# Kernel tuning notes

Hardware: AMD Instinct MI355X
Metric: run time of the kernel (lower is better)

## Reference

```python
import jax, jax.numpy as jnp
import numpy as np

EMBED_DIM = 256
B, H, S = 8, 20, 1024


def setup_inputs() -> dict:
    key = jax.random.key(0)
    ks = jax.random.split(key, 10)
    E = EMBED_DIM
    d2, d4 = 2 * E, 4 * E

    def lin(kw, kb, out_dim, in_dim):
        bound = 1.0 / np.sqrt(in_dim)
        w = jax.random.uniform(kw, (out_dim, in_dim), minval=-bound, maxval=bound, dtype=jnp.float32)
        b = jax.random.uniform(kb, (out_dim,), minval=-bound, maxval=bound, dtype=jnp.float32)
        return w, b

    wc_w, wc_b = lin(ks[0], ks[1], d2, d2)
    wh_w, wh_b = lin(ks[2], ks[3], d2, d2)
    qt_w, qt_b = lin(ks[4], ks[5], 1, d2)
    wf_w, wf_b = lin(ks[6], ks[7], E, d4)

    hist = jax.random.normal(ks[8], (B, H, S, d2), dtype=jnp.float32)
    cur = jax.random.normal(ks[9], (B, S, d2), dtype=jnp.float32)
    return {
        "wca_history_embeddings": hist,
        "wca_current_embeddings": cur,
        "wc_w": wc_w, "wc_b": wc_b,
        "wh_w": wh_w, "wh_b": wh_b,
        "qt_w": qt_w, "qt_b": qt_b,
        "wf_w": wf_w, "wf_b": wf_b,
    }


def reference(wca_history_embeddings, wca_current_embeddings,
              wc_w, wc_b, wh_w, wh_b, qt_w, qt_b, wf_w, wf_b):
    # hist: [B, H, S, 2E]; cur: [B, S, 2E]
    c_proj = jnp.einsum('bsd,ed->bse', wca_current_embeddings, wc_w) + wc_b   # [B,S,2E]
    h_proj = jnp.einsum('bhsd,ed->bhse', wca_history_embeddings, wh_w) + wh_b  # [B,H,S,2E]
    gate = jax.nn.sigmoid(c_proj[:, None, :, :] + h_proj)                      # [B,H,S,2E]
    # alpha[b,h,s] = qt(gate) -- raw scores, NO softmax (matches original)
    alpha = jnp.einsum('bhse,e->bhs', gate, qt_w[0]) + qt_b[0]                 # [B,H,S]
    # weighted neighbor sum over history dim
    summed = jnp.einsum('bhs,bhsd->bsd', alpha, wca_history_embeddings)        # [B,S,2E]
    fused = jnp.concatenate([wca_current_embeddings, summed], axis=-1)         # [B,S,4E]
    final = jnp.einsum('bsd,ed->bse', fused, wf_w) + wf_b                      # [B,S,E]
    return final
```

## Files before the change

kernel.cpp:

```cpp
#include <hip/hip_runtime.h>
#include <hip/hip_bf16.h>
#include <stdint.h>

static constexpr int Bn = 8, Hn = 20, Sn = 1024, En = 256, D2 = 512, D4 = 1024;
static constexpr int Mall = Bn * Hn * Sn;
static constexpr int BS   = Bn * Sn;

typedef __attribute__((ext_vector_type(8))) short bf16x8;
typedef __attribute__((ext_vector_type(4))) float f32x4;

__device__ __forceinline__ unsigned short f2bf(float f) {
  unsigned int u = __float_as_uint(f);
  u += 0x7FFFu + ((u >> 16) & 1u);
  return (unsigned short)(u >> 16);
}
__device__ __forceinline__ float bf2f(unsigned short u) {
  return __uint_as_float(((unsigned int)u) << 16);
}
__device__ __forceinline__ float sigmoid_fast(float x) {
  return __builtin_amdgcn_rcpf(1.0f + __expf(-x));
}
__device__ __forceinline__ unsigned int packbf_trunc(float a, float b) {
  return __builtin_amdgcn_perm(__float_as_uint(b), __float_as_uint(a),
                               0x07060302u);
}
__device__ __forceinline__ unsigned int packbf_rne(float a, float b) {
  return ((unsigned int)f2bf(b) << 16) | (unsigned int)f2bf(a);
}
__device__ __forceinline__ uint4 pack8_trunc(float4 f0, float4 f1) {
  uint4 p;
  p.x = packbf_trunc(f0.x, f0.y);
  p.y = packbf_trunc(f0.z, f0.w);
  p.z = packbf_trunc(f1.x, f1.y);
  p.w = packbf_trunc(f1.z, f1.w);
  return p;
}

typedef const __attribute__((address_space(1))) void gv_t;
typedef __attribute__((address_space(3))) void lv_t;
__device__ __forceinline__ void gload_lds16(const void* g, void* l) {
  __builtin_amdgcn_global_load_lds((gv_t*)g, (lv_t*)l, 16, 0, 0);
}

__global__ __launch_bounds__(256) void k_convert_weights(
    const float* __restrict__ wc, const float* __restrict__ wh,
    const float* __restrict__ wf,
    unsigned short* __restrict__ wcb, unsigned short* __restrict__ whb,
    unsigned short* __restrict__ wfb) {
  int idx4 = blockIdx.x * 256 + threadIdx.x;
  int a = idx4 >> 16;
  int r = idx4 & 65535;
  const float* s = (a == 0) ? wc : (a == 1) ? wh : wf;
  unsigned short* d = (a == 0) ? wcb : (a == 1) ? whb : wfb;
  float4 v = reinterpret_cast<const float4*>(s)[r];
  ushort4 o;
  o.x = f2bf(v.x); o.y = f2bf(v.y); o.z = f2bf(v.z); o.w = f2bf(v.w);
  reinterpret_cast<ushort4*>(d)[r] = o;
}

template <int MODE>
__global__ __launch_bounds__(256) void k_gemm_bt(
    const float* __restrict__ A,
    const unsigned short* __restrict__ Bw,
    const float* __restrict__ bias,
    const unsigned short* __restrict__ cproj,
    const float* __restrict__ qtw,
    const float* __restrict__ qtb,
    unsigned short* __restrict__ cproj_out,
    float* __restrict__ alpha_out) {
  __shared__ __align__(16) unsigned char ldsA[128 * 128];
  __shared__ __align__(16) unsigned char ldsB[128 * 128];

  const int tid = threadIdx.x;
  const int lane = tid & 63, wave = tid >> 6;
  const int lrow = lane & 15, lk = lane >> 4;
  const int row0 = blockIdx.x * 128;
  const f32x4 zero4 = {0.f, 0.f, 0.f, 0.f};

  float asum[2][4];
  if (MODE == 1) {
#pragma unroll
    for (int rf = 0; rf < 2; ++rf)
#pragma unroll
      for (int r = 0; r < 4; ++r) asum[rf][r] = 0.f;
  }

  const int nc_begin = (MODE == 0) ? blockIdx.y : 0;
  const int nc_end   = (MODE == 0) ? (int)blockIdx.y + 1 : 4;

  for (int nc = nc_begin; nc < nc_end; ++nc) {
    f32x4 acc[2][8];
#pragma unroll
    for (int rf = 0; rf < 2; ++rf)
#pragma unroll
      for (int cf = 0; cf < 8; ++cf) acc[rf][cf] = zero4;

    for (int kt = 0; kt < 8; ++kt) {
      __syncthreads();
#pragma unroll
      for (int slot = 0; slot < 4; ++slot) {
        int idx = (slot * 256 + tid) * 8;
        int row = idx >> 6, k = idx & 63;
        const float* src = A + (size_t)(row0 + row) * 512 + kt * 64 + k;
        float4 f0 = *reinterpret_cast<const float4*>(src);
        float4 f1 = *reinterpret_cast<const float4*>(src + 4);
        uint4 p = pack8_trunc(f0, f1);
        int off = row * 128 + ((k * 2) ^ ((row & 7) << 4));
        *reinterpret_cast<uint4*>(ldsA + off) = p;
      }
#pragma unroll
      for (int c = 0; c < 4; ++c) {
        int ci = c * 256 + tid;
        int n = ci >> 3, kc = (ci & 7) * 8;
        const unsigned short* src =
            Bw + (size_t)(nc * 128 + n) * 512 + kt * 64 + kc;
        uint4 p = *reinterpret_cast<const uint4*>(src);
        int off = n * 128 + ((kc * 2) ^ ((n & 7) << 4));
        *reinterpret_cast<uint4*>(ldsB + off) = p;
      }
      __syncthreads();
#pragma unroll
      for (int ks = 0; ks < 2; ++ks) {
        int kbyte = ks * 64 + lk * 16;
        bf16x8 af[2];
#pragma unroll
        for (int rf = 0; rf < 2; ++rf) {
          int ar = wave * 32 + rf * 16 + lrow;
          af[rf] = *reinterpret_cast<const bf16x8*>(
              ldsA + ar * 128 + (kbyte ^ ((ar & 7) << 4)));
        }
#pragma unroll
        for (int cf = 0; cf < 8; ++cf) {
          int br = cf * 16 + lrow;
          bf16x8 bf = *reinterpret_cast<const bf16x8*>(
              ldsB + br * 128 + (kbyte ^ ((br & 7) << 4)));
#pragma unroll
          for (int rf = 0; rf < 2; ++rf)
            acc[rf][cf] = __builtin_amdgcn_mfma_f32_16x16x32_bf16(
                af[rf], bf, acc[rf][cf], 0, 0, 0);
        }
      }
    }

    if (MODE == 0) {
#pragma unroll
      for (int cf = 0; cf < 8; ++cf) {
        int e = nc * 128 + cf * 16 + lrow;
        float bse = bias[e];
#pragma unroll
        for (int rf = 0; rf < 2; ++rf)
#pragma unroll
          for (int r = 0; r < 4; ++r) {
            int row = row0 + wave * 32 + rf * 16 + lk * 4 + r;
            cproj_out[(size_t)row * 512 + e] = f2bf(acc[rf][cf][r] + bse);
          }
      }
    } else {
#pragma unroll
      for (int cf = 0; cf < 8; ++cf) {
        int e = nc * 128 + cf * 16 + lrow;
        float whb = bias[e];
        float qw = qtw[e];
#pragma unroll
        for (int rf = 0; rf < 2; ++rf)
#pragma unroll
          for (int r = 0; r < 4; ++r) {
            int row = row0 + wave * 32 + rf * 16 + lk * 4 + r;
            int bsrow = ((row / (Hn * Sn)) << 10) | (row & 1023);
            float cp = bf2f(cproj[(size_t)bsrow * 512 + e]);
            float g = sigmoid_fast(acc[rf][cf][r] + whb + cp);
            asum[rf][r] = fmaf(g, qw, asum[rf][r]);
          }
      }
    }
  }

  if (MODE == 1) {
#pragma unroll
    for (int off = 1; off < 16; off <<= 1) {
#pragma unroll
      for (int rf = 0; rf < 2; ++rf)
#pragma unroll
        for (int r = 0; r < 4; ++r)
          asum[rf][r] += __shfl_xor(asum[rf][r], off, 64);
    }
    if (lrow == 0) {
      float qb = qtb[0];
#pragma unroll
      for (int rf = 0; rf < 2; ++rf)
#pragma unroll
        for (int r = 0; r < 4; ++r) {
          int row = row0 + wave * 32 + rf * 16 + lk * 4 + r;
          alpha_out[row] = asum[rf][r] + qb;
        }
    }
  }
}

__global__ __launch_bounds__(256, 1) void k_alpha_summed(
    const float* __restrict__ A,
    const unsigned short* __restrict__ Bw,
    const float* __restrict__ bias,
    const unsigned short* __restrict__ cproj,
    const float* __restrict__ qtw,
    const float* __restrict__ qtb,
    unsigned short* __restrict__ summed) {
  __shared__ __align__(16) unsigned char ldsA[81920];
  __shared__ __align__(16) unsigned char ldsB[65536];
  __shared__ __align__(16) unsigned char ldsC[4096];

  const int tid = threadIdx.x;
  const int lane = tid & 63, wave = tid >> 6;
  const int lrow = lane & 15, lk = lane >> 4;
  const int wc = wave;
  const int b = blockIdx.x >> 8;
  const int s0 = (blockIdx.x & 255) * 4;
  const size_t rowbase = (size_t)b * 20480;
  const f32x4 zero4 = {0.f, 0.f, 0.f, 0.f};

  float4 pa[5];
  auto issueA = [&](int sl) {
#pragma unroll
    for (int j = 0; j < 5; ++j) {
      int f = j * 256 + tid;
      int mr = f >> 4, q = f & 15;
      pa[j] = *reinterpret_cast<const float4*>(
          A + (rowbase + (size_t)(mr >> 2) * 1024 + s0 + (mr & 3)) * 512 +
          sl * 64 + q * 4);
    }
  };
  auto writeA = [&](int sl) {
#pragma unroll
    for (int j = 0; j < 5; ++j) {
      int f = j * 256 + tid;
      int mr = f >> 4, q = f & 15;
      unsigned int u0 = packbf_rne(pa[j].x, pa[j].y);
      unsigned int u1 = packbf_rne(pa[j].z, pa[j].w);
      int g = sl * 8 + (q >> 1);
      int off = mr * 1024 + ((g ^ (mr & 7)) << 4) + ((q & 1) << 3);
      *reinterpret_cast<uint2*>(ldsA + off) = make_uint2(u0, u1);
    }
  };

  const int brow = tid >> 3;
  const int bslot = (tid & 7) ^ (brow & 7);
  const unsigned short* gB0 = Bw + (size_t)brow * 512 + bslot * 8;
  char* lB = (char*)ldsB + wave * 1024;

  {
    const unsigned short* csrc = cproj + ((size_t)b * 1024 + s0) * 512;
    gload_lds16(csrc + tid * 8, (char*)ldsC + wave * 1024);
  }
  issueA(0); writeA(0);
  issueA(1); writeA(1);

  f32x4 acc[5][8];
#pragma unroll
  for (int tm = 0; tm < 5; ++tm)
#pragma unroll
    for (int n = 0; n < 8; ++n) acc[tm][n] = zero4;

  for (int kt = 0; kt < 8; ++kt) {
    __syncthreads();
#pragma unroll
    for (int j = 0; j < 16; ++j)
      gload_lds16(gB0 + j * 16384 + kt * 64, lB + j * 4096);
    __builtin_amdgcn_sched_barrier(0);
    if (kt < 6) {
      issueA(kt + 2);
      __builtin_amdgcn_sched_barrier(0);
      asm volatile("s_waitcnt vmcnt(5)" ::: "memory");
    } else {
      asm volatile("s_waitcnt vmcnt(0)" ::: "memory");
    }
    __builtin_amdgcn_s_barrier();
    __builtin_amdgcn_sched_barrier(0);
#pragma unroll
    for (int ks = 0; ks < 2; ++ks) {
      bf16x8 af[5];
#pragma unroll
      for (int tm = 0; tm < 5; ++tm) {
        int r = tm * 16 + lrow;
        int g = (kt * 8 + ks * 4 + lk) ^ (r & 7);
        af[tm] = *reinterpret_cast<const bf16x8*>(ldsA + r * 1024 + g * 16);
      }
#pragma unroll
      for (int n = 0; n < 8; ++n) {
        int r = wc * 128 + n * 16 + lrow;
        int slot = (ks * 4 + lk) ^ (r & 7);
        bf16x8 bv =
            *reinterpret_cast<const bf16x8*>(ldsB + r * 128 + slot * 16);
#pragma unroll
        for (int tm = 0; tm < 5; ++tm)
          acc[tm][n] = __builtin_amdgcn_mfma_f32_16x16x32_bf16(af[tm], bv,
                                                               acc[tm][n], 0,
                                                               0, 0);
      }
    }
    if (kt < 6) writeA(kt + 2);
  }

  float asum[5][4];
#pragma unroll
  for (int tm = 0; tm < 5; ++tm)
#pragma unroll
    for (int r = 0; r < 4; ++r) asum[tm][r] = 0.f;

  const unsigned short* cpl = reinterpret_cast<const unsigned short*>(ldsC);
#pragma unroll
  for (int n = 0; n < 8; ++n) {
    int e = wc * 128 + n * 16 + lrow;
    float whb = bias[e];
    float qw = qtw[e];
    float cpv[4];
#pragma unroll
    for (int si = 0; si < 4; ++si) cpv[si] = bf2f(cpl[si * 512 + e]);
#pragma unroll
    for (int tm = 0; tm < 5; ++tm)
#pragma unroll
      for (int r = 0; r < 4; ++r) {
        float g = sigmoid_fast(acc[tm][n][r] + whb + cpv[r]);
        asum[tm][r] = fmaf(g, qw, asum[tm][r]);
      }
  }
#pragma unroll
  for (int off = 1; off < 16; off <<= 1)
#pragma unroll
    for (int tm = 0; tm < 5; ++tm)
#pragma unroll
      for (int r = 0; r < 4; ++r)
        asum[tm][r] += __shfl_xor(asum[tm][r], off, 64);

  __syncthreads();
  float* red = reinterpret_cast<float*>(ldsC);
  if (lrow == 0) {
#pragma unroll
    for (int tm = 0; tm < 5; ++tm)
#pragma unroll
      for (int r = 0; r < 4; ++r)
        red[wc * 80 + tm * 16 + lk * 4 + r] = asum[tm][r];
  }
  __syncthreads();

  const int si = wave;
  const float qb = qtb[0];
  float o[8];
#pragma unroll
  for (int j = 0; j < 8; ++j) o[j] = 0.f;
#pragma unroll
  for (int h = 0; h < 20; ++h) {
    int mr = h * 4 + si;
    float a = red[mr] + red[80 + mr] + red[160 + mr] + red[240 + mr] + qb;
    int g = lane ^ (mr & 7);
    bf16x8 av = *reinterpret_cast<const bf16x8*>(ldsA + mr * 1024 + g * 16);
#pragma unroll
    for (int j = 0; j < 8; ++j)
      o[j] = fmaf(a, bf2f((unsigned short)av[j]), o[j]);
  }
  uint4 pk;
  pk.x = packbf_rne(o[0], o[1]);
  pk.y = packbf_rne(o[2], o[3]);
  pk.z = packbf_rne(o[4], o[5]);
  pk.w = packbf_rne(o[6], o[7]);
  size_t orow = (size_t)b * 1024 + s0 + si;
  reinterpret_cast<uint4*>(summed)[orow * 64 + lane] = pk;
}

__global__ __launch_bounds__(256) void k_summed(
    const float* __restrict__ hist, const float* __restrict__ alpha,
    unsigned short* __restrict__ summed) {
  int idx = blockIdx.x * 256 + threadIdx.x;
  int bs = idx >> 7, c4 = idx & 127;
  int b = bs >> 10, s = bs & 1023;
  const float4* hp = reinterpret_cast<const float4*>(hist);
  float4 acc = make_float4(0.f, 0.f, 0.f, 0.f);
#pragma unroll
  for (int h = 0; h < Hn; ++h) {
    int bh = b * Hn + h;
    float a = alpha[(bh << 10) + s];
    float4 v = hp[(size_t)(bh * 1024 + s) * 128 + c4];
    acc.x = fmaf(a, v.x, acc.x);
    acc.y = fmaf(a, v.y, acc.y);
    acc.z = fmaf(a, v.z, acc.z);
    acc.w = fmaf(a, v.w, acc.w);
  }
  ushort4 o;
  o.x = f2bf(acc.x); o.y = f2bf(acc.y); o.z = f2bf(acc.z); o.w = f2bf(acc.w);
  reinterpret_cast<ushort4*>(summed)[idx] = o;
}

__global__ __launch_bounds__(256) void k_final(
    const float* __restrict__ cur,
    const unsigned short* __restrict__ summed,
    const unsigned short* __restrict__ wfb16,
    const float* __restrict__ wf_bias,
    float* __restrict__ out) {
  __shared__ __align__(16) unsigned char ldsA[64 * 128];
  __shared__ __align__(16) unsigned char ldsB[128 * 128];
  const int tid = threadIdx.x;
  const int lane = tid & 63, wave = tid >> 6;
  const int lrow = lane & 15, lk = lane >> 4;
  const int row0 = blockIdx.x * 64;
  const int n0 = blockIdx.y * 128;
  const f32x4 zero4 = {0.f, 0.f, 0.f, 0.f};

  f32x4 acc[8];
#pragma unroll
  for (int cf = 0; cf < 8; ++cf) acc[cf] = zero4;

  for (int kt = 0; kt < 16; ++kt) {
    __syncthreads();
#pragma unroll
    for (int slot = 0; slot < 2; ++slot) {
      int idx = (slot * 256 + tid) * 8;
      int row = idx >> 6, k = idx & 63;
      int gcol = kt * 64 + k;
      uint4 p;
      if (kt < 8) {
        const float* src = cur + (size_t)(row0 + row) * 512 + gcol;
        float4 f0 = *reinterpret_cast<const float4*>(src);
        float4 f1 = *reinterpret_cast<const float4*>(src + 4);
        p = pack8_trunc(f0, f1);
      } else {
        p = *reinterpret_cast<const uint4*>(
            summed + (size_t)(row0 + row) * 512 + gcol - 512);
      }
      int off = row * 128 + ((k * 2) ^ ((row & 7) << 4));
      *reinterpret_cast<uint4*>(ldsA + off) = p;
    }
#pragma unroll
    for (int c = 0; c < 4; ++c) {
      int ci = c * 256 + tid;
      int n = ci >> 3, kc = (ci & 7) * 8;
      uint4 p = *reinterpret_cast<const uint4*>(
          wfb16 + (size_t)(n0 + n) * 1024 + kt * 64 + kc);
      int off = n * 128 + ((kc * 2) ^ ((n & 7) << 4));
      *reinterpret_cast<uint4*>(ldsB + off) = p;
    }
    __syncthreads();
#pragma unroll
    for (int ks = 0; ks < 2; ++ks) {
      int kbyte = ks * 64 + lk * 16;
      int ar = wave * 16 + lrow;
      bf16x8 a = *reinterpret_cast<const bf16x8*>(
          ldsA + ar * 128 + (kbyte ^ ((ar & 7) << 4)));
#pragma unroll
      for (int cf = 0; cf < 8; ++cf) {
        int br = cf * 16 + lrow;
        bf16x8 b = *reinterpret_cast<const bf16x8*>(
            ldsB + br * 128 + (kbyte ^ ((br & 7) << 4)));
        acc[cf] = __builtin_amdgcn_mfma_f32_16x16x32_bf16(a, b, acc[cf], 0, 0, 0);
      }
    }
  }
#pragma unroll
  for (int cf = 0; cf < 8; ++cf) {
    int col = n0 + cf * 16 + lrow;
    float bse = wf_bias[col];
#pragma unroll
    for (int r = 0; r < 4; ++r) {
      int row = row0 + wave * 16 + lk * 4 + r;
      out[(size_t)row * 256 + col] = acc[cf][r] + bse;
    }
  }
}

extern "C" void kernel_launch(void* const* d_in, const int* in_sizes, int n_in,
                              void* d_out, int out_size, void* d_ws,
                              size_t ws_size, hipStream_t stream) {
  (void)in_sizes; (void)n_in; (void)out_size;
  const float* hist = (const float*)d_in[0];
  const float* cur  = (const float*)d_in[1];
  const float* wc_w = (const float*)d_in[2];
  const float* wc_b = (const float*)d_in[3];
  const float* wh_w = (const float*)d_in[4];
  const float* wh_b = (const float*)d_in[5];
  const float* qt_w = (const float*)d_in[6];
  const float* qt_b = (const float*)d_in[7];
  const float* wf_w = (const float*)d_in[8];
  const float* wf_b = (const float*)d_in[9];
  float* out = (float*)d_out;
  char* ws = (char*)d_ws;

  unsigned short* wcb    = (unsigned short*)(ws);
  unsigned short* whb    = (unsigned short*)(ws + 524288);
  unsigned short* wfb    = (unsigned short*)(ws + 1048576);
  unsigned short* cproj  = (unsigned short*)(ws + 1572864);
  float*          alpha  = (float*)(ws + 9961472);
  unsigned short* summed = (unsigned short*)(ws + 10616832);
  const size_t NEED = 19005440;

  k_convert_weights<<<dim3(768), dim3(256), 0, stream>>>(wc_w, wh_w, wf_w, wcb,
                                                         whb, wfb);
  k_gemm_bt<0><<<dim3(BS / 128, 4), dim3(256), 0, stream>>>(
      cur, wcb, wc_b, nullptr, nullptr, nullptr, cproj, nullptr);
  if (ws_size >= NEED) {
    k_alpha_summed<<<dim3(2048), dim3(256), 0, stream>>>(
        hist, whb, wh_b, cproj, qt_w, qt_b, summed);
  } else {
    k_gemm_bt<1><<<dim3(Mall / 128, 1), dim3(256), 0, stream>>>(
        hist, whb, wh_b, cproj, qt_w, qt_b, nullptr, alpha);
    k_summed<<<dim3(4096), dim3(256), 0, stream>>>(hist, alpha, summed);
  }
  k_final<<<dim3(BS / 64, 2), dim3(256), 0, stream>>>(cur, summed, wfb, wf_b,
                                                      out);
}
```

Before: 273.2 us.

## Split fused alpha kernel across eight waves with double-buffered half-K weight pipeline

The fused alpha/summed kernel goes from 256 to 512 threads. Each of the eight waves now owns 64 output columns instead of 128. The weight tile is staged in 32-wide K slices into a double-buffered LDS region, and the loop is unrolled into 16 explicit steps with hand-tuned vmcnt waits that interleave the next weight and history loads with compute. The goal is better latency hiding and more waves to overlap global loads with MFMA, at the cost of twice as many barriers and a wider cross-wave reduction over eight partial sums.

```diff
diff --git a/kernel.cpp b/kernel.cpp
--- a/kernel.cpp
+++ b/kernel.cpp
@@ -197,7 +197,7 @@
   }
 }
 
-__global__ __launch_bounds__(256, 1) void k_alpha_summed(
+__global__ __launch_bounds__(512, 2) void k_alpha_summed(
     const float* __restrict__ A,
     const unsigned short* __restrict__ Bw,
     const float* __restrict__ bias,
@@ -218,98 +218,124 @@
   const size_t rowbase = (size_t)b * 20480;
   const f32x4 zero4 = {0.f, 0.f, 0.f, 0.f};
 
-  float4 pa[5];
-  auto issueA = [&](int sl) {
-#pragma unroll
-    for (int j = 0; j < 5; ++j) {
-      int f = j * 256 + tid;
-      int mr = f >> 4, q = f & 15;
-      pa[j] = *reinterpret_cast<const float4*>(
-          A + (rowbase + (size_t)(mr >> 2) * 1024 + s0 + (mr & 3)) * 512 +
-          sl * 64 + q * 4);
+  const unsigned short* gB0 =
+      Bw + (size_t)(lane >> 2) * 512 + ((lane & 3) ^ ((lane >> 3) & 3)) * 8;
+
+  float4 paA[3], paB[3];
+  auto issueA = [&](int t, float4 (&pa)[3]) {
+#pragma unroll
+    for (int j = 0; j < 3; ++j) {
+      if (j < 2 || tid < 256) {
+        int u = j * 512 + tid;
+        int mr = u >> 4, q = u & 15;
+        pa[j] = *reinterpret_cast<const float4*>(
+            A + (rowbase + (size_t)(mr >> 2) * 1024 + s0 + (mr & 3)) * 512 +
+            t * 64 + q * 4);
+      }
     }
   };
-  auto writeA = [&](int sl) {
-#pragma unroll
-    for (int j = 0; j < 5; ++j) {
-      int f = j * 256 + tid;
-      int mr = f >> 4, q = f & 15;
-      unsigned int u0 = packbf_rne(pa[j].x, pa[j].y);
-      unsigned int u1 = packbf_rne(pa[j].z, pa[j].w);
-      int g = sl * 8 + (q >> 1);
-      int off = mr * 1024 + ((g ^ (mr & 7)) << 4) + ((q & 1) << 3);
-      *reinterpret_cast<uint2*>(ldsA + off) = make_uint2(u0, u1);
+  auto writeA = [&](int t, float4 (&pa)[3]) {
+#pragma unroll
+    for (int j = 0; j < 3; ++j) {
+      if (j < 2 || tid < 256) {
+        int u = j * 512 + tid;
+        int mr = u >> 4, q = u & 15;
+        unsigned int u0 = packbf_rne(pa[j].x, pa[j].y);
+        unsigned int u1 = packbf_rne(pa[j].z, pa[j].w);
+        int g = t * 8 + (q >> 1);
+        int off = mr * 1024 + ((g ^ (mr & 7)) << 4) + ((q & 1) << 3);
+        *reinterpret_cast<uint2*>(ldsA + off) = make_uint2(u0, u1);
+      }
     }
   };
-
-  const int brow = tid >> 3;
-  const int bslot = (tid & 7) ^ (brow & 7);
-  const unsigned short* gB0 = Bw + (size_t)brow * 512 + bslot * 8;
-  char* lB = (char*)ldsB + wave * 1024;
-
-  {
+  auto issueB = [&](int t) {
+#pragma unroll
+    for (int j = 0; j < 4; ++j)
+      gload_lds16(gB0 + (size_t)(j * 8 + wave) * 8192 + t * 32,
+                  (char*)ldsB + (t & 1) * 32768 + (j * 8 + wave) * 1024);
+  };
+
+  f32x4 acc[5][4];
+#pragma unroll
+  for (int tm = 0; tm < 5; ++tm)
+#pragma unroll
+    for (int n = 0; n < 4; ++n) acc[tm][n] = zero4;
+
+  auto compute = [&](int k) {
+    const int kt = k >> 1, ks = k & 1;
+    bf16x8 af[5];
+#pragma unroll
+    for (int tm = 0; tm < 5; ++tm) {
+      int r = tm * 16 + lrow;
+      int g = (kt * 8 + ks * 4 + lk) ^ (r & 7);
+      af[tm] = *reinterpret_cast<const bf16x8*>(ldsA + r * 1024 + g * 16);
+    }
+    const unsigned char* bbase = ldsB + (k & 1) * 32768;
+#pragma unroll
+    for (int n = 0; n < 4; ++n) {
+      int r = wc * 64 + n * 16 + lrow;
+      int slot = lk ^ ((r >> 1) & 3);
+      bf16x8 bv = *reinterpret_cast<const bf16x8*>(bbase + r * 64 + slot * 16);
+#pragma unroll
+      for (int tm = 0; tm < 5; ++tm)
+        acc[tm][n] = __builtin_amdgcn_mfma_f32_16x16x32_bf16(af[tm], bv,
+                                                             acc[tm][n], 0, 0,
+                                                             0);
+    }
+  };
+
+  if (wave < 4) {
     const unsigned short* csrc = cproj + ((size_t)b * 1024 + s0) * 512;
     gload_lds16(csrc + tid * 8, (char*)ldsC + wave * 1024);
   }
-  issueA(0); writeA(0);
-  issueA(1); writeA(1);
-
-  f32x4 acc[5][8];
+  issueA(0, paA);
+  issueA(1, paB);
+  writeA(0, paA);
+  writeA(1, paB);
+  issueB(0);
+  issueB(1);
+  issueA(2, paA);
+
+#define KSTEP(K, VM, ...)                                        \
+  {                                                              \
+    asm volatile("s_waitcnt " VM ::: "memory");                  \
+    __builtin_amdgcn_s_barrier();                                \
+    __builtin_amdgcn_sched_barrier(0);                           \
+    compute(K);                                                  \
+    asm volatile("s_waitcnt lgkmcnt(0)" ::: "memory");           \
+    __builtin_amdgcn_s_barrier();                                \
+    __builtin_amdgcn_sched_barrier(0);                           \
+    __VA_ARGS__                                                  \
+  }
+
+  KSTEP(0, "vmcnt(6) lgkmcnt(0)", issueB(2); issueA(3, paB);)
+  KSTEP(1, "vmcnt(8)",  issueB(3);  writeA(2, paA);)
+  KSTEP(2, "vmcnt(6)",  issueB(4);  issueA(4, paA);)
+  KSTEP(3, "vmcnt(6)",  issueB(5);  writeA(3, paB);)
+  KSTEP(4, "vmcnt(6)",  issueB(6);  issueA(5, paB);)
+  KSTEP(5, "vmcnt(6)",  issueB(7);  writeA(4, paA);)
+  KSTEP(6, "vmcnt(6)",  issueB(8);  issueA(6, paA);)
+  KSTEP(7, "vmcnt(6)",  issueB(9);  writeA(5, paB);)
+  KSTEP(8, "vmcnt(6)",  issueB(10); issueA(7, paB);)
+  KSTEP(9, "vmcnt(6)",  issueB(11); writeA(6, paA);)
+  KSTEP(10, "vmcnt(6)", issueB(12);)
+  KSTEP(11, "vmcnt(4)", issueB(13); writeA(7, paB);)
+  KSTEP(12, "vmcnt(4)", issueB(14);)
+  KSTEP(13, "vmcnt(4)", issueB(15);)
+  KSTEP(14, "vmcnt(4)", )
+  KSTEP(15, "vmcnt(0)", )
+#undef KSTEP
+
+  float asum[5][4];
 #pragma unroll
   for (int tm = 0; tm < 5; ++tm)
 #pragma unroll
-    for (int n = 0; n < 8; ++n) acc[tm][n] = zero4;
-
-  for (int kt = 0; kt < 8; ++kt) {
-    __syncthreads();
-#pragma unroll
-    for (int j = 0; j < 16; ++j)
-      gload_lds16(gB0 + j * 16384 + kt * 64, lB + j * 4096);
-    __builtin_amdgcn_sched_barrier(0);
-    if (kt < 6) {
-      issueA(kt + 2);
-      __builtin_amdgcn_sched_barrier(0);
-      asm volatile("s_waitcnt vmcnt(5)" ::: "memory");
-    } else {
-      asm volatile("s_waitcnt vmcnt(0)" ::: "memory");
-    }
-    __builtin_amdgcn_s_barrier();
-    __builtin_amdgcn_sched_barrier(0);
-#pragma unroll
-    for (int ks = 0; ks < 2; ++ks) {
-      bf16x8 af[5];
-#pragma unroll
-      for (int tm = 0; tm < 5; ++tm) {
-        int r = tm * 16 + lrow;
-        int g = (kt * 8 + ks * 4 + lk) ^ (r & 7);
-        af[tm] = *reinterpret_cast<const bf16x8*>(ldsA + r * 1024 + g * 16);
-      }
-#pragma unroll
-      for (int n = 0; n < 8; ++n) {
-        int r = wc * 128 + n * 16 + lrow;
-        int slot = (ks * 4 + lk) ^ (r & 7);
-        bf16x8 bv =
-            *reinterpret_cast<const bf16x8*>(ldsB + r * 128 + slot * 16);
-#pragma unroll
-        for (int tm = 0; tm < 5; ++tm)
-          acc[tm][n] = __builtin_amdgcn_mfma_f32_16x16x32_bf16(af[tm], bv,
-                                                               acc[tm][n], 0,
-                                                               0, 0);
-      }
-    }
-    if (kt < 6) writeA(kt + 2);
-  }
-
-  float asum[5][4];
-#pragma unroll
-  for (int tm = 0; tm < 5; ++tm)
-#pragma unroll
     for (int r = 0; r < 4; ++r) asum[tm][r] = 0.f;
 
   const unsigned short* cpl = reinterpret_cast<const unsigned short*>(ldsC);
 #pragma unroll
-  for (int n = 0; n < 8; ++n) {
-    int e = wc * 128 + n * 16 + lrow;
+  for (int n = 0; n < 4; ++n) {
+    int e = wc * 64 + n * 16 + lrow;
     float whb = bias[e];
     float qw = qtw[e];
     float cpv[4];
@@ -331,8 +357,7 @@
       for (int r = 0; r < 4; ++r)
         asum[tm][r] += __shfl_xor(asum[tm][r], off, 64);
 
-  __syncthreads();
-  float* red = reinterpret_cast<float*>(ldsC);
+  float* red = reinterpret_cast<float*>(ldsB);
   if (lrow == 0) {
 #pragma unroll
     for (int tm = 0; tm < 5; ++tm)
@@ -342,28 +367,32 @@
   }
   __syncthreads();
 
-  const int si = wave;
-  const float qb = qtb[0];
-  float o[8];
-#pragma unroll
-  for (int j = 0; j < 8; ++j) o[j] = 0.f;
-#pragma unroll
-  for (int h = 0; h < 20; ++h) {
-    int mr = h * 4 + si;
-    float a = red[mr] + red[80 + mr] + red[160 + mr] + red[240 + mr] + qb;
-    int g = lane ^ (mr & 7);
-    bf16x8 av = *reinterpret_cast<const bf16x8*>(ldsA + mr * 1024 + g * 16);
-#pragma unroll
-    for (int j = 0; j < 8; ++j)
-      o[j] = fmaf(a, bf2f((unsigned short)av[j]), o[j]);
-  }
-  uint4 pk;
-  pk.x = packbf_rne(o[0], o[1]);
-  pk.y = packbf_rne(o[2], o[3]);
-  pk.z = packbf_rne(o[4], o[5]);
-  pk.w = packbf_rne(o[6], o[7]);
-  size_t orow = (size_t)b * 1024 + s0 + si;
-  reinterpret_cast<uint4*>(summed)[orow * 64 + lane] = pk;
+  if (wave < 4) {
+    const int si = wave;
+    const float qb = qtb[0];
+    float o[8];
+#pragma unroll
+    for (int j = 0; j < 8; ++j) o[j] = 0.f;
+#pragma unroll
+    for (int h = 0; h < 20; ++h) {
+      int mr = h * 4 + si;
+      float a = qb;
+#pragma unroll
+      for (int wq = 0; wq < 8; ++wq) a += red[wq * 80 + mr];
+      int g = lane ^ (mr & 7);
+      bf16x8 av = *reinterpret_cast<const bf16x8*>(ldsA + mr * 1024 + g * 16);
+#pragma unroll
+      for (int j = 0; j < 8; ++j)
+        o[j] = fmaf(a, bf2f((unsigned short)av[j]), o[j]);
+    }
+    uint4 pk;
+    pk.x = packbf_rne(o[0], o[1]);
+    pk.y = packbf_rne(o[2], o[3]);
+    pk.z = packbf_rne(o[4], o[5]);
+    pk.w = packbf_rne(o[6], o[7]);
+    size_t orow = (size_t)b * 1024 + s0 + si;
+    reinterpret_cast<uint4*>(summed)[orow * 64 + lane] = pk;
+  }
 }
 
 __global__ __launch_bounds__(256) void k_summed(
@@ -495,7 +524,7 @@
   k_gemm_bt<0><<<dim3(BS / 128, 4), dim3(256), 0, stream>>>(
       cur, wcb, wc_b, nullptr, nullptr, nullptr, cproj, nullptr);
   if (ws_size >= NEED) {
-    k_alpha_summed<<<dim3(2048), dim3(256), 0, stream>>>(
+    k_alpha_summed<<<dim3(2048), dim3(512), 0, stream>>>(
         hist, whb, wh_b, cproj, qt_w, qt_b, summed);
   } else {
     k_gemm_bt<1><<<dim3(Mall / 128, 1), dim3(256), 0, stream>>>(
```

Result: faster. 239.7 us (-12.3%).

## Use eight waves per block in alpha_summed with per-wave double-buffered weight tiles

Applied to the files above, without the earlier changes.

Doubles the k_alpha_summed block to 512 threads, so each wave owns 64 of the 512 projection columns instead of 128. The whole 80-row history tile is converted and staged into LDS up front. The weight matrix is then streamed in 32-wide k slices, double-buffered per wave, which removes the block-wide barrier from the k-loop. The aim is more waves to hide latency and a lighter MFMA accumulator footprint per wave. The cost is that history loading is no longer overlapped with the GEMM inside a block, and LDS usage likely still limits residency to one block per CU despite the launch bound of 2.

```diff
diff --git a/kernel.cpp b/kernel.cpp
--- a/kernel.cpp
+++ b/kernel.cpp
@@ -197,7 +197,7 @@
   }
 }
 
-__global__ __launch_bounds__(256, 1) void k_alpha_summed(
+__global__ __launch_bounds__(512, 2) void k_alpha_summed(
     const float* __restrict__ A,
     const unsigned short* __restrict__ Bw,
     const float* __restrict__ bias,
@@ -218,86 +218,93 @@
   const size_t rowbase = (size_t)b * 20480;
   const f32x4 zero4 = {0.f, 0.f, 0.f, 0.f};
 
-  float4 pa[5];
-  auto issueA = [&](int sl) {
+  const unsigned short* gB0 =
+      Bw + (size_t)(wave * 64 + (lane >> 2)) * 512 +
+      ((lane & 3) ^ ((lane >> 3) & 3)) * 8;
+
+  auto issueB = [&](int k) {
+#pragma unroll
+    for (int j = 0; j < 4; ++j)
+      gload_lds16(gB0 + (size_t)j * 8192 + k * 32,
+                  (char*)ldsB + (k & 1) * 32768 + wave * 4096 + j * 1024);
+  };
+
+  float4 pa0[5], pa1[5];
+  auto issueA = [&](int bt, float4 (&pa)[5]) {
 #pragma unroll
     for (int j = 0; j < 5; ++j) {
-      int f = j * 256 + tid;
-      int mr = f >> 4, q = f & 15;
+      int u = (bt * 5 + j) * 512 + tid;
+      int mr = u >> 7, c4 = u & 127;
       pa[j] = *reinterpret_cast<const float4*>(
           A + (rowbase + (size_t)(mr >> 2) * 1024 + s0 + (mr & 3)) * 512 +
-          sl * 64 + q * 4);
+          c4 * 4);
     }
   };
-  auto writeA = [&](int sl) {
+  auto writeA = [&](int bt, float4 (&pa)[5]) {
 #pragma unroll
     for (int j = 0; j < 5; ++j) {
-      int f = j * 256 + tid;
-      int mr = f >> 4, q = f & 15;
+      int u = (bt * 5 + j) * 512 + tid;
+      int mr = u >> 7, c4 = u & 127;
       unsigned int u0 = packbf_rne(pa[j].x, pa[j].y);
       unsigned int u1 = packbf_rne(pa[j].z, pa[j].w);
-      int g = sl * 8 + (q >> 1);
-      int off = mr * 1024 + ((g ^ (mr & 7)) << 4) + ((q & 1) << 3);
+      int off = mr * 1024 + (((c4 >> 1) ^ (mr & 7)) << 4) + ((c4 & 1) << 3);
       *reinterpret_cast<uint2*>(ldsA + off) = make_uint2(u0, u1);
     }
   };
 
-  const int brow = tid >> 3;
-  const int bslot = (tid & 7) ^ (brow & 7);
-  const unsigned short* gB0 = Bw + (size_t)brow * 512 + bslot * 8;
-  char* lB = (char*)ldsB + wave * 1024;
-
-  {
+  if (wave < 4) {
     const unsigned short* csrc = cproj + ((size_t)b * 1024 + s0) * 512;
     gload_lds16(csrc + tid * 8, (char*)ldsC + wave * 1024);
   }
-  issueA(0); writeA(0);
-  issueA(1); writeA(1);
-
-  f32x4 acc[5][8];
+  issueA(0, pa0);
+  issueA(1, pa1);
+  writeA(0, pa0);
+  issueA(2, pa0);
+  writeA(1, pa1);
+  issueA(3, pa1);
+  writeA(2, pa0);
+  writeA(3, pa1);
+  issueB(0);
+  issueB(1);
+  __syncthreads();
+
+  f32x4 acc[5][4];
 #pragma unroll
   for (int tm = 0; tm < 5; ++tm)
 #pragma unroll
-    for (int n = 0; n < 8; ++n) acc[tm][n] = zero4;
-
-  for (int kt = 0; kt < 8; ++kt) {
-    __syncthreads();
-#pragma unroll
-    for (int j = 0; j < 16; ++j)
-      gload_lds16(gB0 + j * 16384 + kt * 64, lB + j * 4096);
+    for (int n = 0; n < 4; ++n) acc[tm][n] = zero4;
+
+#pragma unroll 4
+  for (int k = 0; k < 16; ++k) {
+    bf16x8 af[5];
+#pragma unroll
+    for (int tm = 0; tm < 5; ++tm) {
+      int r = tm * 16 + lrow;
+      int g = (k * 4 + lk) ^ (r & 7);
+      af[tm] = *reinterpret_cast<const bf16x8*>(ldsA + r * 1024 + g * 16);
+    }
+    const unsigned char* bbase = ldsB + (k & 1) * 32768 + wave * 4096;
+#pragma unroll
+    for (int n = 0; n < 4; ++n) {
+      int rl = n * 16 + lrow;
+      int slot = lk ^ ((rl >> 1) & 3);
+      bf16x8 bv = *reinterpret_cast<const bf16x8*>(bbase + rl * 64 + slot * 16);
+#pragma unroll
+      for (int tm = 0; tm < 5; ++tm)
+        acc[tm][n] = __builtin_amdgcn_mfma_f32_16x16x32_bf16(af[tm], bv,
+                                                             acc[tm][n], 0, 0,
+                                                             0);
+    }
+    asm volatile("s_waitcnt lgkmcnt(0)" ::: "memory");
     __builtin_amdgcn_sched_barrier(0);
-    if (kt < 6) {
-      issueA(kt + 2);
+    if (k < 14) {
+      issueB(k + 2);
       __builtin_amdgcn_sched_barrier(0);
-      asm volatile("s_waitcnt vmcnt(5)" ::: "memory");
-    } else {
+      asm volatile("s_waitcnt vmcnt(4)" ::: "memory");
+    } else if (k == 14) {
       asm volatile("s_waitcnt vmcnt(0)" ::: "memory");
     }
-    __builtin_amdgcn_s_barrier();
     __builtin_amdgcn_sched_barrier(0);
-#pragma unroll
-    for (int ks = 0; ks < 2; ++ks) {
-      bf16x8 af[5];
-#pragma unroll
-      for (int tm = 0; tm < 5; ++tm) {
-        int r = tm * 16 + lrow;
-        int g = (kt * 8 + ks * 4 + lk) ^ (r & 7);
-        af[tm] = *reinterpret_cast<const bf16x8*>(ldsA + r * 1024 + g * 16);
-      }
-#pragma unroll
-      for (int n = 0; n < 8; ++n) {
-        int r = wc * 128 + n * 16 + lrow;
-        int slot = (ks * 4 + lk) ^ (r & 7);
-        bf16x8 bv =
-            *reinterpret_cast<const bf16x8*>(ldsB + r * 128 + slot * 16);
-#pragma unroll
-        for (int tm = 0; tm < 5; ++tm)
-          acc[tm][n] = __builtin_amdgcn_mfma_f32_16x16x32_bf16(af[tm], bv,
-                                                               acc[tm][n], 0,
-                                                               0, 0);
-      }
-    }
-    if (kt < 6) writeA(kt + 2);
   }
 
   float asum[5][4];
@@ -308,8 +315,8 @@
 
   const unsigned short* cpl = reinterpret_cast<const unsigned short*>(ldsC);
 #pragma unroll
-  for (int n = 0; n < 8; ++n) {
-    int e = wc * 128 + n * 16 + lrow;
+  for (int n = 0; n < 4; ++n) {
+    int e = wc * 64 + n * 16 + lrow;
     float whb = bias[e];
     float qw = qtw[e];
     float cpv[4];
@@ -332,7 +339,7 @@
         asum[tm][r] += __shfl_xor(asum[tm][r], off, 64);
 
   __syncthreads();
-  float* red = reinterpret_cast<float*>(ldsC);
+  float* red = reinterpret_cast<float*>(ldsB);
   if (lrow == 0) {
 #pragma unroll
     for (int tm = 0; tm < 5; ++tm)
@@ -342,28 +349,32 @@
   }
   __syncthreads();
 
-  const int si = wave;
-  const float qb = qtb[0];
-  float o[8];
-#pragma unroll
-  for (int j = 0; j < 8; ++j) o[j] = 0.f;
-#pragma unroll
-  for (int h = 0; h < 20; ++h) {
-    int mr = h * 4 + si;
-    float a = red[mr] + red[80 + mr] + red[160 + mr] + red[240 + mr] + qb;
-    int g = lane ^ (mr & 7);
-    bf16x8 av = *reinterpret_cast<const bf16x8*>(ldsA + mr * 1024 + g * 16);
-#pragma unroll
-    for (int j = 0; j < 8; ++j)
-      o[j] = fmaf(a, bf2f((unsigned short)av[j]), o[j]);
-  }
-  uint4 pk;
-  pk.x = packbf_rne(o[0], o[1]);
-  pk.y = packbf_rne(o[2], o[3]);
-  pk.z = packbf_rne(o[4], o[5]);
-  pk.w = packbf_rne(o[6], o[7]);
-  size_t orow = (size_t)b * 1024 + s0 + si;
-  reinterpret_cast<uint4*>(summed)[orow * 64 + lane] = pk;
+  if (wave < 4) {
+    const int si = wave;
+    const float qb = qtb[0];
+    float o[8];
+#pragma unroll
+    for (int j = 0; j < 8; ++j) o[j] = 0.f;
+#pragma unroll
+    for (int h = 0; h < 20; ++h) {
+      int mr = h * 4 + si;
+      float a = qb;
+#pragma unroll
+      for (int wq = 0; wq < 8; ++wq) a += red[wq * 80 + mr];
+      int g = lane ^ (mr & 7);
+      bf16x8 av = *reinterpret_cast<const bf16x8*>(ldsA + mr * 1024 + g * 16);
+#pragma unroll
+      for (int j = 0; j < 8; ++j)
+        o[j] = fmaf(a, bf2f((unsigned short)av[j]), o[j]);
+    }
+    uint4 pk;
+    pk.x = packbf_rne(o[0], o[1]);
+    pk.y = packbf_rne(o[2], o[3]);
+    pk.z = packbf_rne(o[4], o[5]);
+    pk.w = packbf_rne(o[6], o[7]);
+    size_t orow = (size_t)b * 1024 + s0 + si;
+    reinterpret_cast<uint4*>(summed)[orow * 64 + lane] = pk;
+  }
 }
 
 __global__ __launch_bounds__(256) void k_summed(
@@ -495,7 +506,7 @@
   k_gemm_bt<0><<<dim3(BS / 128, 4), dim3(256), 0, stream>>>(
       cur, wcb, wc_b, nullptr, nullptr, nullptr, cproj, nullptr);
   if (ws_size >= NEED) {
-    k_alpha_summed<<<dim3(2048), dim3(256), 0, stream>>>(
+    k_alpha_summed<<<dim3(2048), dim3(512), 0, stream>>>(
         hist, whb, wh_b, cproj, qt_w, qt_b, summed);
   } else {
     k_gemm_bt<1><<<dim3(Mall / 128, 1), dim3(256), 0, stream>>>(
```

Result: faster. 223.0 us (-18.4%).
